# Optimization experiments

Hardware: AMD Instinct MI355X
Metric: run time of the kernel (lower is better)

Reference implementation:

```python
import jax, jax.numpy as jnp
import numpy as np

IN_FEATURES = 4096
OUT_FEATURES = 4096
RANK = 16
SCALING = 1.0  # lora_alpha / r = 16 / 16


def setup_inputs() -> dict:
    key = jax.random.key(0)
    k1, k2, k3, k4 = jax.random.split(key, 4)
    x = jax.random.normal(k1, (4, 2048, IN_FEATURES), dtype=jnp.float32)
    # packed weight: (out_features, in_features // 4), repeated x4 at forward time
    weight_packed = jax.random.normal(k2, (OUT_FEATURES, IN_FEATURES // 4), dtype=jnp.float32) * 0.02
    lora_A = jax.random.normal(k3, (RANK, IN_FEATURES), dtype=jnp.float32) * 0.02
    lora_B = jax.random.normal(k4, (OUT_FEATURES, RANK), dtype=jnp.float32) * 0.02
    return {"x": x, "weight_packed": weight_packed, "lora_A": lora_A, "lora_B": lora_B, "scaling": 1}


def reference(x, weight_packed, lora_A, lora_B, scaling):
    W = jnp.tile(weight_packed, (1, 4))  # [out, in]
    base = jnp.einsum('bsi,oi->bso', x, W)
    # LoRA low-rank path: (x @ A^T) @ B^T * scaling
    lora = jnp.einsum('bsr,or->bso', jnp.einsum('bsi,ri->bsr', x, lora_A), lora_B)
    return base + lora * jnp.float32(scaling)
```

## Files before the change

kernel.cpp:

```cpp
#include <hip/hip_runtime.h>
#include <hip/hip_bf16.h>
#include <stdint.h>

#define M_DIM 8192
#define N_DIM 4096
#define K_DIM 4096
#define RANK  16

#define BM 256
#define BN 256
#define BK 64
#define NKT (K_DIM / BK)

typedef __attribute__((ext_vector_type(8))) __bf16 bf16x8;
typedef __attribute__((ext_vector_type(4))) float  f32x4;

__device__ __forceinline__ unsigned short f2bf(float f) {
    union { float f; uint32_t u; } c; c.f = f;
    uint32_t b = c.u;
    b += 0x7FFFu + ((b >> 16) & 1u);
    return (unsigned short)(b >> 16);
}

__global__ void convert_x_kernel(const float* __restrict__ x,
                                 unsigned short* __restrict__ xb, int n4) {
    int idx = blockIdx.x * blockDim.x + threadIdx.x;
    int stride = gridDim.x * blockDim.x;
    for (int i = idx; i < n4; i += stride) {
        float4 v = reinterpret_cast<const float4*>(x)[i];
        ushort4 o;
        o.x = f2bf(v.x); o.y = f2bf(v.y); o.z = f2bf(v.z); o.w = f2bf(v.w);
        reinterpret_cast<ushort4*>(xb)[i] = o;
    }
}

__global__ void build_weff_kernel(const float* __restrict__ wp,
                                  const float* __restrict__ lA,
                                  const float* __restrict__ lB,
                                  const int*   __restrict__ scaling,
                                  unsigned short* __restrict__ weff) {
    int o = blockIdx.x;
    float s = (float)scaling[0];
    float b[RANK];
#pragma unroll
    for (int r = 0; r < RANK; ++r) b[r] = lB[o * RANK + r] * s;
    int tid = threadIdx.x;
#pragma unroll
    for (int ii = 0; ii < 16; ++ii) {
        int i = tid + ii * 256;
        float acc = wp[o * 1024 + (i & 1023)];
#pragma unroll
        for (int r = 0; r < RANK; ++r) acc = fmaf(b[r], lA[r * 4096 + i], acc);
        weff[(size_t)o * 4096 + i] = f2bf(acc);
    }
}


template<int MH, int NH>
__device__ __forceinline__ void mfma_quad(const bf16x8 (&a)[4][2], const bf16x8 (&b)[2][2],
                                          f32x4 (&acc)[8][4]) {
#pragma unroll
    for (int kc = 0; kc < 2; ++kc)
#pragma unroll
        for (int mf = 0; mf < 4; ++mf)
#pragma unroll
            for (int nf = 0; nf < 2; ++nf)
                acc[MH * 4 + mf][NH * 2 + nf] = __builtin_amdgcn_mfma_f32_16x16x32_bf16(
                    a[mf][kc], b[nf][kc], acc[MH * 4 + mf][NH * 2 + nf], 0, 0, 0);
}

__global__ __launch_bounds__(512, 2) void gemm_kernel(
    const unsigned short* __restrict__ A,
    const unsigned short* __restrict__ B,
    float* __restrict__ C)
{
    __shared__ __align__(16) char lds[131072];

    const int tid  = threadIdx.x;
    const int lane = tid & 63;
    const int wave = tid >> 6;
    const int wr = wave >> 2;
    const int wc = wave & 3;

    const int bid = blockIdx.x;
    const int swz = (bid & 7) * 64 + (bid >> 3);
    const int bm = swz >> 4;
    const int bn = swz & 15;
    const int m0 = bm * BM;
    const int n0 = bn * BN;

    const int srccol = 8 * ((tid & 7) ^ ((tid >> 3) & 7));
    const int wub    = (tid & ~63) * 16;
    const unsigned short* Ag = A + (size_t)(m0 + (tid >> 3)) * K_DIM + srccol;
    const unsigned short* Bg = B + (size_t)(n0 + (tid >> 8) * 64 + ((tid >> 3) & 31)) * K_DIM + srccol;

#define STAGE_A(buf, mh, kt) do { \
    __builtin_amdgcn_global_load_lds( \
        (const __attribute__((address_space(1))) void*)(Ag + (size_t)((mh) * 64) * K_DIM + (size_t)(kt) * 64), \
        (__attribute__((address_space(3))) void*)(lds + (buf) * 65536 + (mh) * 16384 + wub), 16, 0, 0); \
    __builtin_amdgcn_global_load_lds( \
        (const __attribute__((address_space(1))) void*)(Ag + (size_t)(128 + (mh) * 64) * K_DIM + (size_t)(kt) * 64), \
        (__attribute__((address_space(3))) void*)(lds + (buf) * 65536 + (mh) * 16384 + 8192 + wub), 16, 0, 0); \
} while (0)

#define STAGE_B(buf, nh, kt) do { \
    __builtin_amdgcn_global_load_lds( \
        (const __attribute__((address_space(1))) void*)(Bg + (size_t)((nh) * 32) * K_DIM + (size_t)(kt) * 64), \
        (__attribute__((address_space(3))) void*)(lds + (buf) * 65536 + 32768 + (nh) * 16384 + wub), 16, 0, 0); \
    __builtin_amdgcn_global_load_lds( \
        (const __attribute__((address_space(1))) void*)(Bg + (size_t)(128 + (nh) * 32) * K_DIM + (size_t)(kt) * 64), \
        (__attribute__((address_space(3))) void*)(lds + (buf) * 65536 + 32768 + (nh) * 16384 + 8192 + wub), 16, 0, 0); \
} while (0)

    const int wrA   = wr * 8192;
    const int wcB   = wc * 4096;
    const int rdrow = (lane & 15) * 128;
    const int rdxor = (lane & 7) << 4;
    const int rdg   = (lane >> 4) * 16;

#define RD_A(dst, buf, mh) do { \
    _Pragma("unroll") for (int mf = 0; mf < 4; ++mf) \
    _Pragma("unroll") for (int kc = 0; kc < 2; ++kc) \
        dst[mf][kc] = *(const bf16x8*)(lds + (buf) * 65536 + (mh) * 16384 + wrA + rdrow + mf * 2048 + ((kc * 64 + rdg) ^ rdxor)); \
} while (0)

#define RD_B(dst, buf, nh) do { \
    _Pragma("unroll") for (int nf = 0; nf < 2; ++nf) \
    _Pragma("unroll") for (int kc = 0; kc < 2; ++kc) \
        dst[nf][kc] = *(const bf16x8*)(lds + (buf) * 65536 + 32768 + (nh) * 16384 + wcB + rdrow + nf * 2048 + ((kc * 64 + rdg) ^ rdxor)); \
} while (0)

#define PH_TAIL(QUAD) \
    __builtin_amdgcn_s_barrier(); \
    asm volatile("s_waitcnt lgkmcnt(0)" ::: "memory"); \
    __builtin_amdgcn_s_setprio(1); \
    QUAD; \
    __builtin_amdgcn_s_setprio(0);

    f32x4 acc[8][4];
#pragma unroll
    for (int i = 0; i < 8; ++i)
#pragma unroll
        for (int j = 0; j < 4; ++j) acc[i][j] = (f32x4){0.f, 0.f, 0.f, 0.f};

    bf16x8 afr[4][2];
    bf16x8 bfr[2][2];

    STAGE_A(0, 0, 0); STAGE_B(0, 1, 0); STAGE_A(0, 1, 0); STAGE_B(0, 0, 0);
    STAGE_A(1, 0, 1); STAGE_B(1, 1, 1);
    asm volatile("s_waitcnt vmcnt(4)" ::: "memory");
    __builtin_amdgcn_s_barrier();

    for (int it = 0; it < NKT / 2; ++it) {
        const int k1 = 2 * it + 1;
        const int k2 = (2 * it + 2) & (NKT - 1);
        const int k3 = (2 * it + 3) & (NKT - 1);

        RD_A(afr, 0, 0); RD_B(bfr, 0, 0);
        STAGE_A(1, 1, k1);
        PH_TAIL((mfma_quad<0, 0>(afr, bfr, acc)));
        __builtin_amdgcn_s_barrier();
        RD_B(bfr, 0, 1);
        STAGE_B(1, 0, k1);
        PH_TAIL((mfma_quad<0, 1>(afr, bfr, acc)));
        __builtin_amdgcn_s_barrier();
        RD_A(afr, 0, 1);
        STAGE_A(0, 0, k2);
        PH_TAIL((mfma_quad<1, 1>(afr, bfr, acc)));
        __builtin_amdgcn_s_barrier();
        RD_B(bfr, 0, 0);
        STAGE_B(0, 1, k2);
        PH_TAIL((mfma_quad<1, 0>(afr, bfr, acc)));
        asm volatile("s_waitcnt vmcnt(4)" ::: "memory");
        __builtin_amdgcn_s_barrier();
        RD_A(afr, 1, 0); RD_B(bfr, 1, 0);
        STAGE_A(0, 1, k2);
        PH_TAIL((mfma_quad<0, 0>(afr, bfr, acc)));
        __builtin_amdgcn_s_barrier();
        RD_B(bfr, 1, 1);
        STAGE_B(0, 0, k2);
        PH_TAIL((mfma_quad<0, 1>(afr, bfr, acc)));
        __builtin_amdgcn_s_barrier();
        RD_A(afr, 1, 1);
        STAGE_A(1, 0, k3);
        PH_TAIL((mfma_quad<1, 1>(afr, bfr, acc)));
        __builtin_amdgcn_s_barrier();
        RD_B(bfr, 1, 0);
        STAGE_B(1, 1, k3);
        PH_TAIL((mfma_quad<1, 0>(afr, bfr, acc)));
        asm volatile("s_waitcnt vmcnt(4)" ::: "memory");
        __builtin_amdgcn_s_barrier();
    }

    const int crow = m0 + wr * 128 + (lane >> 4) * 4;
    const int ccol = n0 + wc * 64 + (lane & 15);
#pragma unroll
    for (int mi = 0; mi < 8; ++mi)
#pragma unroll
        for (int ni = 0; ni < 4; ++ni)
#pragma unroll
            for (int r = 0; r < 4; ++r)
                C[(size_t)(crow + mi * 16 + r) * N_DIM + ccol + ni * 16] = acc[mi][ni][r];

#undef STAGE_A
#undef STAGE_B
#undef RD_A
#undef RD_B
#undef PH_TAIL
}

extern "C" void kernel_launch(void* const* d_in, const int* in_sizes, int n_in,
                              void* d_out, int out_size, void* d_ws, size_t ws_size,
                              hipStream_t stream) {
    const float* x  = (const float*)d_in[0];
    const float* wp = (const float*)d_in[1];
    const float* lA = (const float*)d_in[2];
    const float* lB = (const float*)d_in[3];
    const int*   sc = (const int*)d_in[4];
    float* out = (float*)d_out;

    unsigned short* xb   = (unsigned short*)d_ws;
    unsigned short* weff = (unsigned short*)d_ws + (size_t)M_DIM * K_DIM;

    convert_x_kernel<<<2048, 256, 0, stream>>>(x, xb, (M_DIM * K_DIM) / 4);
    build_weff_kernel<<<N_DIM, 256, 0, stream>>>(wp, lA, lB, sc, weff);

    int grid = (M_DIM / BM) * (N_DIM / BN);
    gemm_kernel<<<grid, 512, 0, stream>>>(xb, weff, out);
}
```

Measured before the change: 332.4 us.

## Switch GEMM to 32x32x16 MFMA and fuse prep kernels into one launch

The GEMM inner loop now uses 32x32x16 bf16 MFMA tiles instead of 16x16x32. The LDS fragment reads and the output store mapping are reworked to match, and two B fragment buffers are kept so some repeated LDS reads are dropped. The x conversion and weight-building kernels are merged into one launch, with wider 8-element conversion stores. This aims to cut LDS traffic and instruction count per MFMA and to remove one launch. In exchange it raises register pressure and makes the fragment-to-swizzle mapping harder to verify.

```diff
diff --git a/kernel.cpp b/kernel.cpp
--- a/kernel.cpp
+++ b/kernel.cpp
@@ -12,8 +12,9 @@
 #define BK 64
 #define NKT (K_DIM / BK)
 
-typedef __attribute__((ext_vector_type(8))) __bf16 bf16x8;
-typedef __attribute__((ext_vector_type(4))) float  f32x4;
+typedef __attribute__((ext_vector_type(8)))  __bf16 bf16x8;
+typedef __attribute__((ext_vector_type(16))) float  f32x16;
+typedef __attribute__((ext_vector_type(8)))  unsigned short u16x8;
 
 __device__ __forceinline__ unsigned short f2bf(float f) {
     union { float f; uint32_t u; } c; c.f = f;
@@ -22,51 +23,55 @@
     return (unsigned short)(b >> 16);
 }
 
-__global__ void convert_x_kernel(const float* __restrict__ x,
-                                 unsigned short* __restrict__ xb, int n4) {
-    int idx = blockIdx.x * blockDim.x + threadIdx.x;
-    int stride = gridDim.x * blockDim.x;
-    for (int i = idx; i < n4; i += stride) {
-        float4 v = reinterpret_cast<const float4*>(x)[i];
-        ushort4 o;
-        o.x = f2bf(v.x); o.y = f2bf(v.y); o.z = f2bf(v.z); o.w = f2bf(v.w);
-        reinterpret_cast<ushort4*>(xb)[i] = o;
+#define CONV_BLOCKS 2048
+__global__ __launch_bounds__(256) void prep_kernel(
+    const float* __restrict__ x,
+    const float* __restrict__ wp,
+    const float* __restrict__ lA,
+    const float* __restrict__ lB,
+    const int*   __restrict__ scaling,
+    unsigned short* __restrict__ xb,
+    unsigned short* __restrict__ weff) {
+    const int tid = threadIdx.x;
+    if (blockIdx.x < N_DIM) {
+        int o = blockIdx.x;
+        float s = (float)scaling[0];
+        float b[RANK];
+#pragma unroll
+        for (int r = 0; r < RANK; ++r) b[r] = lB[o * RANK + r] * s;
+#pragma unroll
+        for (int ii = 0; ii < 16; ++ii) {
+            int i = tid + ii * 256;
+            float acc = wp[o * 1024 + (i & 1023)];
+#pragma unroll
+            for (int r = 0; r < RANK; ++r) acc = fmaf(b[r], lA[r * 4096 + i], acc);
+            weff[(size_t)o * 4096 + i] = f2bf(acc);
+        }
+    } else {
+        const int n8 = (M_DIM * K_DIM) / 8;
+        int idx = (blockIdx.x - N_DIM) * 256 + tid;
+        const int stride = CONV_BLOCKS * 256;
+        for (int i = idx; i < n8; i += stride) {
+            float4 v0 = reinterpret_cast<const float4*>(x)[2 * i];
+            float4 v1 = reinterpret_cast<const float4*>(x)[2 * i + 1];
+            u16x8 o;
+            o[0] = f2bf(v0.x); o[1] = f2bf(v0.y); o[2] = f2bf(v0.z); o[3] = f2bf(v0.w);
+            o[4] = f2bf(v1.x); o[5] = f2bf(v1.y); o[6] = f2bf(v1.z); o[7] = f2bf(v1.w);
+            reinterpret_cast<u16x8*>(xb)[i] = o;
+        }
     }
 }
 
-__global__ void build_weff_kernel(const float* __restrict__ wp,
-                                  const float* __restrict__ lA,
-                                  const float* __restrict__ lB,
-                                  const int*   __restrict__ scaling,
-                                  unsigned short* __restrict__ weff) {
-    int o = blockIdx.x;
-    float s = (float)scaling[0];
-    float b[RANK];
-#pragma unroll
-    for (int r = 0; r < RANK; ++r) b[r] = lB[o * RANK + r] * s;
-    int tid = threadIdx.x;
-#pragma unroll
-    for (int ii = 0; ii < 16; ++ii) {
-        int i = tid + ii * 256;
-        float acc = wp[o * 1024 + (i & 1023)];
-#pragma unroll
-        for (int r = 0; r < RANK; ++r) acc = fmaf(b[r], lA[r * 4096 + i], acc);
-        weff[(size_t)o * 4096 + i] = f2bf(acc);
-    }
-}
-
-
-template<int MH, int NH>
-__device__ __forceinline__ void mfma_quad(const bf16x8 (&a)[4][2], const bf16x8 (&b)[2][2],
-                                          f32x4 (&acc)[8][4]) {
-#pragma unroll
-    for (int kc = 0; kc < 2; ++kc)
-#pragma unroll
-        for (int mf = 0; mf < 4; ++mf)
-#pragma unroll
-            for (int nf = 0; nf < 2; ++nf)
-                acc[MH * 4 + mf][NH * 2 + nf] = __builtin_amdgcn_mfma_f32_16x16x32_bf16(
-                    a[mf][kc], b[nf][kc], acc[MH * 4 + mf][NH * 2 + nf], 0, 0, 0);
+
+template<int MH, int NT>
+__device__ __forceinline__ void mfma_quad(const bf16x8 (&a)[2][4], const bf16x8 (&b)[4],
+                                          f32x16 (&acc)[4][2]) {
+#pragma unroll
+    for (int kc = 0; kc < 4; ++kc)
+#pragma unroll
+        for (int mt = 0; mt < 2; ++mt)
+            acc[MH * 2 + mt][NT] = __builtin_amdgcn_mfma_f32_32x32x16_bf16(
+                a[mt][kc], b[kc], acc[MH * 2 + mt][NT], 0, 0, 0);
 }
 
 __global__ __launch_bounds__(512, 2) void gemm_kernel(
@@ -114,20 +119,19 @@
 
     const int wrA   = wr * 8192;
     const int wcB   = wc * 4096;
-    const int rdrow = (lane & 15) * 128;
+    const int rdrow = (lane & 31) * 128;
     const int rdxor = (lane & 7) << 4;
-    const int rdg   = (lane >> 4) * 16;
+    const int rdg   = (lane >> 5) * 16;
 
 #define RD_A(dst, buf, mh) do { \
-    _Pragma("unroll") for (int mf = 0; mf < 4; ++mf) \
-    _Pragma("unroll") for (int kc = 0; kc < 2; ++kc) \
-        dst[mf][kc] = *(const bf16x8*)(lds + (buf) * 65536 + (mh) * 16384 + wrA + rdrow + mf * 2048 + ((kc * 64 + rdg) ^ rdxor)); \
+    _Pragma("unroll") for (int mt = 0; mt < 2; ++mt) \
+    _Pragma("unroll") for (int kc = 0; kc < 4; ++kc) \
+        dst[mt][kc] = *(const bf16x8*)(lds + (buf) * 65536 + (mh) * 16384 + wrA + mt * 4096 + rdrow + ((kc * 32 + rdg) ^ rdxor)); \
 } while (0)
 
 #define RD_B(dst, buf, nh) do { \
-    _Pragma("unroll") for (int nf = 0; nf < 2; ++nf) \
-    _Pragma("unroll") for (int kc = 0; kc < 2; ++kc) \
-        dst[nf][kc] = *(const bf16x8*)(lds + (buf) * 65536 + 32768 + (nh) * 16384 + wcB + rdrow + nf * 2048 + ((kc * 64 + rdg) ^ rdxor)); \
+    _Pragma("unroll") for (int kc = 0; kc < 4; ++kc) \
+        dst[kc] = *(const bf16x8*)(lds + (buf) * 65536 + 32768 + (nh) * 16384 + wcB + rdrow + ((kc * 32 + rdg) ^ rdxor)); \
 } while (0)
 
 #define PH_TAIL(QUAD) \
@@ -137,14 +141,16 @@
     QUAD; \
     __builtin_amdgcn_s_setprio(0);
 
-    f32x4 acc[8][4];
-#pragma unroll
-    for (int i = 0; i < 8; ++i)
-#pragma unroll
-        for (int j = 0; j < 4; ++j) acc[i][j] = (f32x4){0.f, 0.f, 0.f, 0.f};
-
-    bf16x8 afr[4][2];
-    bf16x8 bfr[2][2];
+    f32x16 acc[4][2];
+#pragma unroll
+    for (int i = 0; i < 4; ++i)
+#pragma unroll
+        for (int j = 0; j < 2; ++j)
+#pragma unroll
+            for (int r = 0; r < 16; ++r) acc[i][j][r] = 0.f;
+
+    bf16x8 afr[2][4];
+    bf16x8 b0[4], b1[4];
 
     STAGE_A(0, 0, 0); STAGE_B(0, 1, 0); STAGE_A(0, 1, 0); STAGE_B(0, 0, 0);
     STAGE_A(1, 0, 1); STAGE_B(1, 1, 1);
@@ -156,51 +162,50 @@
         const int k2 = (2 * it + 2) & (NKT - 1);
         const int k3 = (2 * it + 3) & (NKT - 1);
 
-        RD_A(afr, 0, 0); RD_B(bfr, 0, 0);
+        RD_A(afr, 0, 0); RD_B(b0, 0, 0);
         STAGE_A(1, 1, k1);
-        PH_TAIL((mfma_quad<0, 0>(afr, bfr, acc)));
-        __builtin_amdgcn_s_barrier();
-        RD_B(bfr, 0, 1);
+        PH_TAIL((mfma_quad<0, 0>(afr, b0, acc)));
+        __builtin_amdgcn_s_barrier();
+        RD_B(b1, 0, 1);
         STAGE_B(1, 0, k1);
-        PH_TAIL((mfma_quad<0, 1>(afr, bfr, acc)));
+        PH_TAIL((mfma_quad<0, 1>(afr, b1, acc)));
         __builtin_amdgcn_s_barrier();
         RD_A(afr, 0, 1);
         STAGE_A(0, 0, k2);
-        PH_TAIL((mfma_quad<1, 1>(afr, bfr, acc)));
-        __builtin_amdgcn_s_barrier();
-        RD_B(bfr, 0, 0);
+        PH_TAIL((mfma_quad<1, 1>(afr, b1, acc)));
+        __builtin_amdgcn_s_barrier();
         STAGE_B(0, 1, k2);
-        PH_TAIL((mfma_quad<1, 0>(afr, bfr, acc)));
+        PH_TAIL((mfma_quad<1, 0>(afr, b0, acc)));
         asm volatile("s_waitcnt vmcnt(4)" ::: "memory");
         __builtin_amdgcn_s_barrier();
-        RD_A(afr, 1, 0); RD_B(bfr, 1, 0);
+        RD_A(afr, 1, 0); RD_B(b0, 1, 0);
         STAGE_A(0, 1, k2);
-        PH_TAIL((mfma_quad<0, 0>(afr, bfr, acc)));
-        __builtin_amdgcn_s_barrier();
-        RD_B(bfr, 1, 1);
+        PH_TAIL((mfma_quad<0, 0>(afr, b0, acc)));
+        __builtin_amdgcn_s_barrier();
+        RD_B(b1, 1, 1);
         STAGE_B(0, 0, k2);
-        PH_TAIL((mfma_quad<0, 1>(afr, bfr, acc)));
+        PH_TAIL((mfma_quad<0, 1>(afr, b1, acc)));
         __builtin_amdgcn_s_barrier();
         RD_A(afr, 1, 1);
         STAGE_A(1, 0, k3);
-        PH_TAIL((mfma_quad<1, 1>(afr, bfr, acc)));
-        __builtin_amdgcn_s_barrier();
-        RD_B(bfr, 1, 0);
+        PH_TAIL((mfma_quad<1, 1>(afr, b1, acc)));
+        __builtin_amdgcn_s_barrier();
         STAGE_B(1, 1, k3);
-        PH_TAIL((mfma_quad<1, 0>(afr, bfr, acc)));
+        PH_TAIL((mfma_quad<1, 0>(afr, b0, acc)));
         asm volatile("s_waitcnt vmcnt(4)" ::: "memory");
         __builtin_amdgcn_s_barrier();
     }
 
-    const int crow = m0 + wr * 128 + (lane >> 4) * 4;
-    const int ccol = n0 + wc * 64 + (lane & 15);
-#pragma unroll
-    for (int mi = 0; mi < 8; ++mi)
-#pragma unroll
-        for (int ni = 0; ni < 4; ++ni)
-#pragma unroll
-            for (int r = 0; r < 4; ++r)
-                C[(size_t)(crow + mi * 16 + r) * N_DIM + ccol + ni * 16] = acc[mi][ni][r];
+    const int crow = m0 + wr * 128 + 4 * (lane >> 5);
+    const int ccol = n0 + wc * 64 + (lane & 31);
+#pragma unroll
+    for (int mt = 0; mt < 4; ++mt)
+#pragma unroll
+        for (int nt = 0; nt < 2; ++nt)
+#pragma unroll
+            for (int r = 0; r < 16; ++r)
+                C[(size_t)(crow + mt * 32 + (r & 3) + 8 * (r >> 2)) * N_DIM + ccol + nt * 32] =
+                    acc[mt][nt][r];
 
 #undef STAGE_A
 #undef STAGE_B
@@ -222,8 +227,7 @@
     unsigned short* xb   = (unsigned short*)d_ws;
     unsigned short* weff = (unsigned short*)d_ws + (size_t)M_DIM * K_DIM;
 
-    convert_x_kernel<<<2048, 256, 0, stream>>>(x, xb, (M_DIM * K_DIM) / 4);
-    build_weff_kernel<<<N_DIM, 256, 0, stream>>>(wp, lA, lB, sc, weff);
+    prep_kernel<<<N_DIM + CONV_BLOCKS, 256, 0, stream>>>(x, wp, lA, lB, sc, xb, weff);
 
     int grid = (M_DIM / BM) * (N_DIM / BN);
     gemm_kernel<<<grid, 512, 0, stream>>>(xb, weff, out);
```

After: 403.2 us. 1.21x slower.

## Fuse x conversion and effective-weight build into one prep kernel

Applied to the files above, without the earlier changes.

Merges the x fp32-to-bf16 conversion and the W_eff = tile(W)+B·A build into a single launch. Block ranges split the work: the first range builds W_eff with lora_A tiles staged in LDS and float4 loads, and the second converts x with 8-wide vector stores. This removes one kernel launch, lets the two independent memory-bound jobs overlap, and cuts redundant global reads of lora_A. It also adds an extra partial lgkmcnt wait inside the GEMM loop, which is likely redundant with the full wait that follows.

```diff
diff --git a/kernel.cpp b/kernel.cpp
--- a/kernel.cpp
+++ b/kernel.cpp
@@ -14,6 +14,7 @@
 
 typedef __attribute__((ext_vector_type(8))) __bf16 bf16x8;
 typedef __attribute__((ext_vector_type(4))) float  f32x4;
+typedef __attribute__((ext_vector_type(8))) unsigned short u16x8;
 
 __device__ __forceinline__ unsigned short f2bf(float f) {
     union { float f; uint32_t u; } c; c.f = f;
@@ -22,36 +23,68 @@
     return (unsigned short)(b >> 16);
 }
 
-__global__ void convert_x_kernel(const float* __restrict__ x,
-                                 unsigned short* __restrict__ xb, int n4) {
-    int idx = blockIdx.x * blockDim.x + threadIdx.x;
-    int stride = gridDim.x * blockDim.x;
-    for (int i = idx; i < n4; i += stride) {
-        float4 v = reinterpret_cast<const float4*>(x)[i];
-        ushort4 o;
-        o.x = f2bf(v.x); o.y = f2bf(v.y); o.z = f2bf(v.z); o.w = f2bf(v.w);
-        reinterpret_cast<ushort4*>(xb)[i] = o;
-    }
-}
-
-__global__ void build_weff_kernel(const float* __restrict__ wp,
-                                  const float* __restrict__ lA,
-                                  const float* __restrict__ lB,
-                                  const int*   __restrict__ scaling,
-                                  unsigned short* __restrict__ weff) {
-    int o = blockIdx.x;
-    float s = (float)scaling[0];
-    float b[RANK];
-#pragma unroll
-    for (int r = 0; r < RANK; ++r) b[r] = lB[o * RANK + r] * s;
-    int tid = threadIdx.x;
-#pragma unroll
-    for (int ii = 0; ii < 16; ++ii) {
-        int i = tid + ii * 256;
-        float acc = wp[o * 1024 + (i & 1023)];
-#pragma unroll
-        for (int r = 0; r < RANK; ++r) acc = fmaf(b[r], lA[r * 4096 + i], acc);
-        weff[(size_t)o * 4096 + i] = f2bf(acc);
+#define WEFF_BLOCKS 1024
+#define CONV_BLOCKS 2048
+__global__ __launch_bounds__(256) void prep_kernel(
+    const float* __restrict__ x,
+    const float* __restrict__ wp,
+    const float* __restrict__ lA,
+    const float* __restrict__ lB,
+    const int*   __restrict__ scaling,
+    unsigned short* __restrict__ xb,
+    unsigned short* __restrict__ weff) {
+    __shared__ float lAs[16][512];
+    const int t = threadIdx.x;
+    if (blockIdx.x < WEFF_BLOCKS) {
+        const int bo = blockIdx.x >> 3;
+        const int bi = blockIdx.x & 7;
+#pragma unroll
+        for (int v = 0; v < 8; ++v) {
+            int idx = v * 256 + t;
+            int r = idx >> 7;
+            int c4 = idx & 127;
+            reinterpret_cast<float4*>(&lAs[r][0])[c4] =
+                reinterpret_cast<const float4*>(lA + (size_t)r * 4096 + bi * 512)[c4];
+        }
+        __syncthreads();
+        const int row = t >> 3;
+        const int o = bo * 32 + row;
+        const float s = (float)scaling[0];
+        float b[RANK];
+#pragma unroll
+        for (int r = 0; r < RANK; ++r) b[r] = lB[o * RANK + r] * s;
+        const float* wrow = wp + (size_t)o * 1024;
+        const int cbase = (t & 7) * 4;
+#pragma unroll
+        for (int j = 0; j < 16; ++j) {
+            int c = cbase + j * 32;
+            int gi = bi * 512 + c;
+            float4 w = *reinterpret_cast<const float4*>(wrow + (gi & 1023));
+            float a0 = w.x, a1 = w.y, a2 = w.z, a3 = w.w;
+#pragma unroll
+            for (int r = 0; r < RANK; ++r) {
+                float4 la = *reinterpret_cast<const float4*>(&lAs[r][c]);
+                a0 = fmaf(b[r], la.x, a0);
+                a1 = fmaf(b[r], la.y, a1);
+                a2 = fmaf(b[r], la.z, a2);
+                a3 = fmaf(b[r], la.w, a3);
+            }
+            ushort4 ov;
+            ov.x = f2bf(a0); ov.y = f2bf(a1); ov.z = f2bf(a2); ov.w = f2bf(a3);
+            *reinterpret_cast<ushort4*>(weff + (size_t)o * 4096 + gi) = ov;
+        }
+    } else {
+        const int n8 = (M_DIM * K_DIM) / 8;
+        int idx = (blockIdx.x - WEFF_BLOCKS) * 256 + t;
+        const int stride = CONV_BLOCKS * 256;
+        for (int i = idx; i < n8; i += stride) {
+            float4 v0 = reinterpret_cast<const float4*>(x)[2 * i];
+            float4 v1 = reinterpret_cast<const float4*>(x)[2 * i + 1];
+            u16x8 o;
+            o[0] = f2bf(v0.x); o[1] = f2bf(v0.y); o[2] = f2bf(v0.z); o[3] = f2bf(v0.w);
+            o[4] = f2bf(v1.x); o[5] = f2bf(v1.y); o[6] = f2bf(v1.z); o[7] = f2bf(v1.w);
+            reinterpret_cast<u16x8*>(xb)[i] = o;
+        }
     }
 }
 
@@ -158,6 +191,7 @@
 
         RD_A(afr, 0, 0); RD_B(bfr, 0, 0);
         STAGE_A(1, 1, k1);
+        asm volatile("s_waitcnt lgkmcnt(8)" ::: "memory");
         PH_TAIL((mfma_quad<0, 0>(afr, bfr, acc)));
         __builtin_amdgcn_s_barrier();
         RD_B(bfr, 0, 1);
@@ -175,6 +209,7 @@
         __builtin_amdgcn_s_barrier();
         RD_A(afr, 1, 0); RD_B(bfr, 1, 0);
         STAGE_A(0, 1, k2);
+        asm volatile("s_waitcnt lgkmcnt(8)" ::: "memory");
         PH_TAIL((mfma_quad<0, 0>(afr, bfr, acc)));
         __builtin_amdgcn_s_barrier();
         RD_B(bfr, 1, 1);
@@ -222,8 +257,7 @@
     unsigned short* xb   = (unsigned short*)d_ws;
     unsigned short* weff = (unsigned short*)d_ws + (size_t)M_DIM * K_DIM;
 
-    convert_x_kernel<<<2048, 256, 0, stream>>>(x, xb, (M_DIM * K_DIM) / 4);
-    build_weff_kernel<<<N_DIM, 256, 0, stream>>>(wp, lA, lB, sc, weff);
+    prep_kernel<<<WEFF_BLOCKS + CONV_BLOCKS, 256, 0, stream>>>(x, wp, lA, lB, sc, xb, weff);
 
     int grid = (M_DIM / BM) * (N_DIM / BN);
     gemm_kernel<<<grid, 512, 0, stream>>>(xb, weff, out);
```

Result: faster. 282.8 us (-14.9%).
